# Performance work log

Measured on AMD Instinct MI355X. Metric: run time of the kernel, lower is better.

The kernel has to match this reference:

```python
import jax, jax.numpy as jnp
import numpy as np

DIM = 256
N_EMBED = 1024
COMMITMENT_COST = 0.25


def setup_inputs() -> dict:
    key = jax.random.key(0)
    k1, k2 = jax.random.split(key)
    z = jax.random.normal(k1, (16, DIM, 64, 64), dtype=jnp.float32)
    lim = 1.0 / (2 * N_EMBED)
    embed_w = jax.random.uniform(k2, (N_EMBED, DIM), dtype=jnp.float32,
                                 minval=-lim, maxval=lim)
    return {"z": z, "embed_w": embed_w}


def reference(z, embed_w):
    # z: [B, C, H, W] -> [B, H, W, C]
    zp = jnp.transpose(z, (0, 2, 3, 1))
    B, H, W, C = zp.shape
    zf = zp.reshape(-1, C)  # [N, dim]
    # Squared euclidean distances to each codebook entry: [N, n_embed]
    d = (jnp.sum(zf * zf, axis=1, keepdims=True)
         + jnp.sum(embed_w * embed_w, axis=1)
         - 2.0 * jnp.matmul(zf, embed_w.T))
    idx = jnp.argmin(d, axis=1)  # [N]
    # Codebook lookup (equivalent to one-hot @ embed_w)
    z_q = embed_w[idx].reshape(zp.shape)  # [B, H, W, C]
    # VQ loss: codebook + commitment terms
    sg = jax.lax.stop_gradient
    loss = (jnp.mean((sg(z_q) - zp) ** 2)
            + COMMITMENT_COST * jnp.mean((z_q - sg(zp)) ** 2))
    # Straight-through estimator
    z_q_st = zp + sg(z_q - zp)
    # Perplexity from code usage histogram
    n = zf.shape[0]
    counts = jax.ops.segment_sum(jnp.ones((n,), jnp.float32), idx,
                                 num_segments=N_EMBED)
    e_mean = counts / n
    perplexity = jnp.exp(-jnp.sum(e_mean * jnp.log(e_mean + 1e-10)))
    z_q_out = jnp.transpose(z_q_st, (0, 3, 1, 2))  # back to [B, C, H, W]
    return loss, z_q_out, idx[:, None], perplexity
```

## Files before the change

kernel.cpp:

```cpp
#include <hip/hip_runtime.h>
#include <hip/hip_bf16.h>

#define BATCH 16
#define CDIM  256
#define HDIM  64
#define WDIM  64
#define NQ    65536
#define NE    1024
#define BM    32
#define KB    32
#define BPAD  260

#define ZQ_OFF   1
#define IDX_OFF  16777217
#define PERP_OFF 16842753

#define WS_EE_OFF    0
#define WS_HIST_OFF  4096
#define WS_LOSS_OFF  8192

__device__ __forceinline__ float pw128_sq(const float* __restrict__ p) {
    float r[8];
#pragma unroll
    for (int j = 0; j < 8; j++) r[j] = __fmul_rn(p[j], p[j]);
#pragma unroll
    for (int i = 8; i < 128; i += 8) {
#pragma unroll
        for (int j = 0; j < 8; j++) r[j] = __fadd_rn(r[j], __fmul_rn(p[i + j], p[i + j]));
    }
    return __fadd_rn(__fadd_rn(__fadd_rn(r[0], r[1]), __fadd_rn(r[2], r[3])),
                     __fadd_rn(__fadd_rn(r[4], r[5]), __fadd_rn(r[6], r[7])));
}

__global__ void vq_prep(const float* __restrict__ W, float* __restrict__ ee,
                        int* __restrict__ hist, double* __restrict__ loss_part) {
    int t = blockIdx.x * 256 + threadIdx.x;
    hist[t] = 0;
    if (t < 256) loss_part[t] = 0.0;
    const float* p = W + (size_t)t * CDIM;
    ee[t] = __fadd_rn(pw128_sq(p), pw128_sq(p + 128));
}

__global__ __launch_bounds__(256, 2)
void vq_argmin(const float* __restrict__ z, const float* __restrict__ W,
               const float* __restrict__ ee, float* __restrict__ out_idx,
               int* __restrict__ hist) {
    __shared__ float A[CDIM][BM];
    __shared__ float Bs[KB][BPAD];
    __shared__ float zz_s[BM];
    __shared__ float tmp2[64];
    __shared__ float pD[BM][8];
    __shared__ int   pI[BM][8];
    float (*redD)[64] = (float (*)[64])(&A[0][0]);
    int   (*redI)[64] = (int   (*)[64])(&A[64][0]);

    const int t   = threadIdx.x;
    const int n0  = blockIdx.x * BM;
    const int b   = n0 >> 12;
    const int h   = (n0 >> 6) & 63;
    const int w0  = n0 & 63;

    const float* zb = z + (size_t)b * (CDIM * HDIM * WDIM) + (size_t)h * WDIM + w0;
#pragma unroll
    for (int v = 0; v < 8; v++) {
        int idx4 = v * 256 + t;
        int c  = idx4 >> 3;
        int w4 = idx4 & 7;
        float4 val = *(const float4*)(zb + (size_t)c * (HDIM * WDIM) + w4 * 4);
        *(float4*)(&A[c][w4 * 4]) = val;
    }
    __syncthreads();

    if (t < 64) {
        int q = t >> 1, base = (t & 1) * 128;
        float r[8];
#pragma unroll
        for (int j = 0; j < 8; j++) { float x = A[base + j][q]; r[j] = __fmul_rn(x, x); }
        for (int i = 8; i < 128; i += 8) {
#pragma unroll
            for (int j = 0; j < 8; j++) { float x = A[base + i + j][q]; r[j] = __fadd_rn(r[j], __fmul_rn(x, x)); }
        }
        tmp2[t] = __fadd_rn(__fadd_rn(__fadd_rn(r[0], r[1]), __fadd_rn(r[2], r[3])),
                            __fadd_rn(__fadd_rn(r[4], r[5]), __fadd_rn(r[6], r[7])));
    }
    __syncthreads();
    if (t < BM) zz_s[t] = __fadd_rn(tmp2[2 * t], tmp2[2 * t + 1]);

    const int tx = t & 63;
    const int ty = t >> 6;
    const int q0 = ty * 8;

    float bestD[8]; int bestI[8];
#pragma unroll
    for (int i = 0; i < 8; i++) { bestD[i] = 3.0e38f; bestI[i] = 0; }

    float4 breg[8];
    {
#pragma unroll
        for (int v = 0; v < 8; v++) {
            int f = v * 256 + t;
            int e = f >> 3, kq = f & 7;
            breg[v] = *(const float4*)(W + (size_t)e * CDIM + kq * 4);
        }
    }

    for (int ec = 0; ec < 4; ec++) {
        const int e0 = ec * 256 + tx * 4;
        float acc[8][4];
#pragma unroll
        for (int i = 0; i < 8; i++)
#pragma unroll
            for (int j = 0; j < 4; j++) acc[i][j] = 0.0f;

        for (int kc = 0; kc < 8; kc++) {
            __syncthreads();
#pragma unroll
            for (int v = 0; v < 8; v++) {
                int f = v * 256 + t;
                int e = f >> 3, kq = f & 7;
                Bs[kq * 4 + 0][e] = breg[v].x;
                Bs[kq * 4 + 1][e] = breg[v].y;
                Bs[kq * 4 + 2][e] = breg[v].z;
                Bs[kq * 4 + 3][e] = breg[v].w;
            }
            int nkc = kc + 1, nec = ec;
            if (nkc == 8) { nkc = 0; nec++; }
            if (nec < 4) {
#pragma unroll
                for (int v = 0; v < 8; v++) {
                    int f = v * 256 + t;
                    int e = f >> 3, kq = f & 7;
                    breg[v] = *(const float4*)(W + (size_t)(nec * 256 + e) * CDIM + nkc * KB + kq * 4);
                }
            }
            __syncthreads();
            const int kb = kc * KB;
#pragma unroll 4
            for (int k = 0; k < KB; k++) {
                const float4 b4 = *(const float4*)(&Bs[k][tx * 4]);
                const float4 a0 = *(const float4*)(&A[kb + k][q0]);
                const float4 a1 = *(const float4*)(&A[kb + k][q0 + 4]);
                float av[8] = {a0.x, a0.y, a0.z, a0.w, a1.x, a1.y, a1.z, a1.w};
                float bv[4] = {b4.x, b4.y, b4.z, b4.w};
#pragma unroll
                for (int i = 0; i < 8; i++)
#pragma unroll
                    for (int j = 0; j < 4; j++)
                        acc[i][j] = __fmaf_rn(av[i], bv[j], acc[i][j]);
            }
        }

        float4 ee4 = *(const float4*)(ee + e0);
        float eev[4] = {ee4.x, ee4.y, ee4.z, ee4.w};
#pragma unroll
        for (int i = 0; i < 8; i++) {
            float zzq = zz_s[q0 + i];
#pragma unroll
            for (int j = 0; j < 4; j++) {
                float s = __fadd_rn(zzq, eev[j]);
                float d = __fsub_rn(s, __fadd_rn(acc[i][j], acc[i][j]));
                if (d < bestD[i]) { bestD[i] = d; bestI[i] = e0 + j; }
            }
        }
    }

    __syncthreads();
#pragma unroll
    for (int i = 0; i < 8; i++) { redD[q0 + i][tx] = bestD[i]; redI[q0 + i][tx] = bestI[i]; }
    __syncthreads();
    {
        int q = t >> 3, s = t & 7;
        float bd = redD[q][s * 8]; int bi = redI[q][s * 8];
#pragma unroll
        for (int u = 1; u < 8; u++) {
            float d2 = redD[q][s * 8 + u]; int i2 = redI[q][s * 8 + u];
            if (d2 < bd || (d2 == bd && i2 < bi)) { bd = d2; bi = i2; }
        }
        pD[q][s] = bd; pI[q][s] = bi;
    }
    __syncthreads();
    if (t < BM) {
        float bd = pD[t][0]; int bi = pI[t][0];
#pragma unroll
        for (int u = 1; u < 8; u++) {
            float d2 = pD[t][u]; int i2 = pI[t][u];
            if (d2 < bd || (d2 == bd && i2 < bi)) { bd = d2; bi = i2; }
        }
        out_idx[n0 + t] = (float)bi;
        atomicAdd(&hist[bi], 1);
    }
}

__global__ void vq_gather(const float* __restrict__ z, const float* __restrict__ W,
                          const float* __restrict__ idxf, float* __restrict__ zq_out,
                          double* __restrict__ loss_part) {
    const int gid = blockIdx.x * 256 + threadIdx.x;
    const int w4 = gid & 15;
    const int r  = gid >> 4;
    const int h  = r & 63;
    const int c  = (r >> 6) & 255;
    const int b  = r >> 14;
    const size_t off = (((size_t)(b * CDIM + c) * HDIM + h) * WDIM) + w4 * 4;
    const float4 zp = *(const float4*)(z + off);
    const int n = b * 4096 + h * 64 + w4 * 4;

    float zpv[4] = {zp.x, zp.y, zp.z, zp.w};
    float ov[4];
    double ls = 0.0;
#pragma unroll
    for (int l = 0; l < 4; l++) {
        int idx = (int)idxf[n + l];
        float zq = W[(size_t)idx * CDIM + c];
        float t1 = __fsub_rn(zq, zpv[l]);
        ov[l] = __fadd_rn(zpv[l], t1);
        ls += (double)t1 * (double)t1;
    }
    float4 o = {ov[0], ov[1], ov[2], ov[3]};
    *(float4*)(zq_out + off) = o;

#pragma unroll
    for (int s = 32; s > 0; s >>= 1) ls += __shfl_down(ls, s, 64);
    __shared__ double wsum[4];
    if ((threadIdx.x & 63) == 0) wsum[threadIdx.x >> 6] = ls;
    __syncthreads();
    if (threadIdx.x == 0) {
        double v = wsum[0] + wsum[1] + wsum[2] + wsum[3];
        atomicAdd(&loss_part[blockIdx.x & 255], v);
    }
}

__global__ void vq_final(const double* __restrict__ loss_part, const int* __restrict__ hist,
                         float* __restrict__ d_out) {
    __shared__ double s1[256], s2[256];
    const int t = threadIdx.x;
    double v = loss_part[t];
    double pv = 0.0;
#pragma unroll
    for (int j = 0; j < 4; j++) {
        int cnt = hist[t * 4 + j];
        double em = (double)cnt / 65536.0;
        pv += em * log(em + 1e-10);
    }
    s1[t] = v; s2[t] = pv;
    __syncthreads();
    for (int st = 128; st > 0; st >>= 1) {
        if (t < st) { s1[t] += s1[t + st]; s2[t] += s2[t + st]; }
        __syncthreads();
    }
    if (t == 0) {
        float m = (float)(s1[0] / 16777216.0);
        d_out[0] = 1.25f * m;
        d_out[PERP_OFF] = (float)exp(-s2[0]);
    }
}

extern "C" void kernel_launch(void* const* d_in, const int* in_sizes, int n_in,
                              void* d_out, int out_size, void* d_ws, size_t ws_size,
                              hipStream_t stream) {
    const float* z = (const float*)d_in[0];
    const float* W = (const float*)d_in[1];
    float* out = (float*)d_out;

    float*  ee        = (float*)((char*)d_ws + WS_EE_OFF);
    int*    hist      = (int*)((char*)d_ws + WS_HIST_OFF);
    double* loss_part = (double*)((char*)d_ws + WS_LOSS_OFF);

    vq_prep<<<4, 256, 0, stream>>>(W, ee, hist, loss_part);
    vq_argmin<<<NQ / BM, 256, 0, stream>>>(z, W, ee, out + IDX_OFF, hist);
    vq_gather<<<(NQ * CDIM / 4) / 256, 256, 0, stream>>>(z, W, out + IDX_OFF, out + ZQ_OFF, loss_part);
    vq_final<<<1, 256, 0, stream>>>(loss_part, hist, out);
}
```

Measured before the change: 640.1 us.

## Pre-transpose codebook and stream it into LDS with async double buffering

```diff
diff --git a/kernel.cpp b/kernel.cpp
--- a/kernel.cpp
+++ b/kernel.cpp
@@ -1,5 +1,4 @@
 #include <hip/hip_runtime.h>
-#include <hip/hip_bf16.h>
 
 #define BATCH 16
 #define CDIM  256
@@ -8,8 +7,7 @@
 #define NQ    65536
 #define NE    1024
 #define BM    32
-#define KB    32
-#define BPAD  260
+#define KB    16
 
 #define ZQ_OFF   1
 #define IDX_OFF  16777217
@@ -18,6 +16,7 @@
 #define WS_EE_OFF    0
 #define WS_HIST_OFF  4096
 #define WS_LOSS_OFF  8192
+#define WS_WT_OFF    16384
 
 __device__ __forceinline__ float pw128_sq(const float* __restrict__ p) {
     float r[8];
@@ -41,24 +40,54 @@
     ee[t] = __fadd_rn(pw128_sq(p), pw128_sq(p + 128));
 }
 
-__global__ __launch_bounds__(256, 2)
-void vq_argmin(const float* __restrict__ z, const float* __restrict__ W,
+__global__ void vq_transpose(const float* __restrict__ W, float* __restrict__ WT) {
+    __shared__ float T[64][65];
+    const int e0 = (blockIdx.x & 15) * 64;
+    const int k0 = (blockIdx.x >> 4) * 64;
+    const int r  = threadIdx.x >> 4;
+    const int c4 = threadIdx.x & 15;
+#pragma unroll
+    for (int s = 0; s < 4; s++) {
+        float4 v = *(const float4*)(W + (size_t)(e0 + s * 16 + r) * CDIM + k0 + c4 * 4);
+        T[s * 16 + r][c4 * 4 + 0] = v.x;
+        T[s * 16 + r][c4 * 4 + 1] = v.y;
+        T[s * 16 + r][c4 * 4 + 2] = v.z;
+        T[s * 16 + r][c4 * 4 + 3] = v.w;
+    }
+    __syncthreads();
+#pragma unroll
+    for (int s = 0; s < 4; s++) {
+        float4 o;
+        o.x = T[c4 * 4 + 0][s * 16 + r];
+        o.y = T[c4 * 4 + 1][s * 16 + r];
+        o.z = T[c4 * 4 + 2][s * 16 + r];
+        o.w = T[c4 * 4 + 3][s * 16 + r];
+        *(float4*)(WT + (size_t)(k0 + s * 16 + r) * NE + e0 + c4 * 4) = o;
+    }
+}
+
+__global__ __launch_bounds__(256, 4)
+void vq_argmin(const float* __restrict__ z, const float* __restrict__ WT,
                const float* __restrict__ ee, float* __restrict__ out_idx,
                int* __restrict__ hist) {
-    __shared__ float A[CDIM][BM];
-    __shared__ float Bs[KB][BPAD];
+    __shared__ __align__(16) float S[8192];
     __shared__ float zz_s[BM];
     __shared__ float tmp2[64];
     __shared__ float pD[BM][8];
     __shared__ int   pI[BM][8];
-    float (*redD)[64] = (float (*)[64])(&A[0][0]);
-    int   (*redI)[64] = (int   (*)[64])(&A[64][0]);
-
-    const int t   = threadIdx.x;
-    const int n0  = blockIdx.x * BM;
-    const int b   = n0 >> 12;
-    const int h   = (n0 >> 6) & 63;
-    const int w0  = n0 & 63;
+
+    float (*A)[BM]       = (float (*)[BM])S;
+    float (*Bs)[KB][256] = (float (*)[KB][256])S;
+    float (*redD)[64]    = (float (*)[64])S;
+    int   (*redI)[64]    = (int (*)[64])(S + 2048);
+
+    const int t    = threadIdx.x;
+    const int lane = t & 63;
+    const int wv   = t >> 6;
+    const int n0   = blockIdx.x * BM;
+    const int b    = n0 >> 12;
+    const int h    = (n0 >> 6) & 63;
+    const int w0   = n0 & 63;
 
     const float* zb = z + (size_t)b * (CDIM * HDIM * WDIM) + (size_t)h * WDIM + w0;
 #pragma unroll
@@ -66,8 +95,7 @@
         int idx4 = v * 256 + t;
         int c  = idx4 >> 3;
         int w4 = idx4 & 7;
-        float4 val = *(const float4*)(zb + (size_t)c * (HDIM * WDIM) + w4 * 4);
-        *(float4*)(&A[c][w4 * 4]) = val;
+        *(float4*)(&A[c][w4 * 4]) = *(const float4*)(zb + (size_t)c * (HDIM * WDIM) + w4 * 4);
     }
     __syncthreads();
 
@@ -86,61 +114,52 @@
     __syncthreads();
     if (t < BM) zz_s[t] = __fadd_rn(tmp2[2 * t], tmp2[2 * t + 1]);
 
-    const int tx = t & 63;
-    const int ty = t >> 6;
-    const int q0 = ty * 8;
+    const int tx  = t & 63;
+    const int q0  = wv * 8;
+    const int q0u = __builtin_amdgcn_readfirstlane(q0);
+    const float* aG = zb + q0u;
+
+    auto stage = [&](int sec, int skc, int nb) {
+#pragma unroll
+        for (int v = 0; v < 4; v++) {
+            const int r_ = v * 4 + wv;
+            const float* g_ = WT + (size_t)(skc * KB + r_) * NE + sec * 256 + lane * 4;
+            __builtin_amdgcn_global_load_lds(
+                (const __attribute__((address_space(1))) void*)g_,
+                (__attribute__((address_space(3))) void*)(&Bs[nb][r_][0]),
+                16, 0, 0);
+        }
+    };
 
     float bestD[8]; int bestI[8];
 #pragma unroll
     for (int i = 0; i < 8; i++) { bestD[i] = 3.0e38f; bestI[i] = 0; }
 
-    float4 breg[8];
-    {
-#pragma unroll
-        for (int v = 0; v < 8; v++) {
-            int f = v * 256 + t;
-            int e = f >> 3, kq = f & 7;
-            breg[v] = *(const float4*)(W + (size_t)e * CDIM + kq * 4);
-        }
-    }
+    stage(0, 0, 0);
+    __syncthreads();
 
     for (int ec = 0; ec < 4; ec++) {
-        const int e0 = ec * 256 + tx * 4;
         float acc[8][4];
 #pragma unroll
         for (int i = 0; i < 8; i++)
 #pragma unroll
             for (int j = 0; j < 4; j++) acc[i][j] = 0.0f;
 
-        for (int kc = 0; kc < 8; kc++) {
-            __syncthreads();
-#pragma unroll
-            for (int v = 0; v < 8; v++) {
-                int f = v * 256 + t;
-                int e = f >> 3, kq = f & 7;
-                Bs[kq * 4 + 0][e] = breg[v].x;
-                Bs[kq * 4 + 1][e] = breg[v].y;
-                Bs[kq * 4 + 2][e] = breg[v].z;
-                Bs[kq * 4 + 3][e] = breg[v].w;
+        for (int kc = 0; kc < 16; kc++) {
+            const int cur = kc & 1;
+            {
+                int nkc = kc + 1, nec = ec;
+                if (nkc == 16) { nkc = 0; nec++; }
+                if (nec < 4) stage(nec, nkc, cur ^ 1);
             }
-            int nkc = kc + 1, nec = ec;
-            if (nkc == 8) { nkc = 0; nec++; }
-            if (nec < 4) {
-#pragma unroll
-                for (int v = 0; v < 8; v++) {
-                    int f = v * 256 + t;
-                    int e = f >> 3, kq = f & 7;
-                    breg[v] = *(const float4*)(W + (size_t)(nec * 256 + e) * CDIM + nkc * KB + kq * 4);
-                }
-            }
-            __syncthreads();
             const int kb = kc * KB;
 #pragma unroll 4
-            for (int k = 0; k < KB; k++) {
-                const float4 b4 = *(const float4*)(&Bs[k][tx * 4]);
-                const float4 a0 = *(const float4*)(&A[kb + k][q0]);
-                const float4 a1 = *(const float4*)(&A[kb + k][q0 + 4]);
-                float av[8] = {a0.x, a0.y, a0.z, a0.w, a1.x, a1.y, a1.z, a1.w};
+            for (int k2 = 0; k2 < KB; k2++) {
+                const float4 b4 = *(const float4*)(&Bs[cur][k2][tx * 4]);
+                const float* ar = aG + (size_t)(kb + k2) * (HDIM * WDIM);
+                float av[8];
+#pragma unroll
+                for (int i = 0; i < 8; i++) av[i] = ar[i];
                 float bv[4] = {b4.x, b4.y, b4.z, b4.w};
 #pragma unroll
                 for (int i = 0; i < 8; i++)
@@ -148,8 +167,10 @@
                     for (int j = 0; j < 4; j++)
                         acc[i][j] = __fmaf_rn(av[i], bv[j], acc[i][j]);
             }
-        }
-
+            __syncthreads();
+        }
+
+        const int e0 = ec * 256 + tx * 4;
         float4 ee4 = *(const float4*)(ee + e0);
         float eev[4] = {ee4.x, ee4.y, ee4.z, ee4.w};
 #pragma unroll
@@ -264,9 +285,11 @@
     float*  ee        = (float*)((char*)d_ws + WS_EE_OFF);
     int*    hist      = (int*)((char*)d_ws + WS_HIST_OFF);
     double* loss_part = (double*)((char*)d_ws + WS_LOSS_OFF);
+    float*  WT        = (float*)((char*)d_ws + WS_WT_OFF);
 
     vq_prep<<<4, 256, 0, stream>>>(W, ee, hist, loss_part);
-    vq_argmin<<<NQ / BM, 256, 0, stream>>>(z, W, ee, out + IDX_OFF, hist);
+    vq_transpose<<<64, 256, 0, stream>>>(W, WT);
+    vq_argmin<<<NQ / BM, 256, 0, stream>>>(z, WT, ee, out + IDX_OFF, hist);
     vq_gather<<<(NQ * CDIM / 4) / 256, 256, 0, stream>>>(z, W, out + IDX_OFF, out + ZQ_OFF, loss_part);
     vq_final<<<1, 256, 0, stream>>>(loss_part, hist, out);
 }
```

New measurement: 556.5 us. 13.1% less time.
